# Kernel optimization log

Measured on AMD Instinct MI355X. Metric: run time of the kernel, lower is better.

## Reference

```python
import jax, jax.numpy as jnp
import numpy as np

RESOLUTION = 2 ** 8  # 256
N_POINTS = 2 ** 21


def setup_inputs() -> dict:
    key = jax.random.key(0)
    k1, k2 = jax.random.split(key)
    inp = jax.random.uniform(k1, (N_POINTS, 3), dtype=jnp.float32)
    grid = jax.random.normal(k2, (RESOLUTION, RESOLUTION, RESOLUTION, 3), dtype=jnp.float32) * 0.01
    return {"input": inp, "feature_params": grid}


def reference(input, feature_params):
    R = feature_params.shape[0]
    scaled = input * (R - 1)
    lower = jnp.clip(jnp.floor(scaled).astype(jnp.int32), 0, R - 2)
    upper = jnp.clip(lower + 1, 0, R - 1)
    t = scaled - lower.astype(scaled.dtype)
    xl, yl, zl = lower[:, 0], lower[:, 1], lower[:, 2]
    xu, yu, zu = upper[:, 0], upper[:, 1], upper[:, 2]
    tx, ty, tz = t[:, 0:1], t[:, 1:2], t[:, 2:3]  # (N,1) for broadcast over channels
    # note original indexes grid as [z, y, x]
    c000 = feature_params[zl, yl, xl]
    c001 = feature_params[zl, yl, xu]
    c010 = feature_params[zl, yu, xl]
    c011 = feature_params[zl, yu, xu]
    c100 = feature_params[zu, yl, xl]
    c101 = feature_params[zu, yl, xu]
    c110 = feature_params[zu, yu, xl]
    c111 = feature_params[zu, yu, xu]
    c00 = c000 * (1 - tx) + c001 * tx
    c01 = c010 * (1 - tx) + c011 * tx
    c10 = c100 * (1 - tx) + c101 * tx
    c11 = c110 * (1 - tx) + c111 * tx
    c0 = c00 * (1 - ty) + c01 * ty
    c1 = c10 * (1 - ty) + c11 * ty
    return c0 * (1 - tz) + c1 * tz
```

## Files before the change

kernel.cpp:

```cpp
#include <hip/hip_runtime.h>


#define NB     8192
#define CAP    512u
#define GBLK   512
#define LAYERF4 1728
#define LAYERF  6912
#define GRIDF4  12582912

#define CUR_OFF   67108864u
#define NEEDED    (67108864u + 32768u)

typedef float f4v __attribute__((ext_vector_type(4)));
typedef float f2v __attribute__((ext_vector_type(2)));
typedef f4v f4u __attribute__((aligned(8)));
typedef f2v f2u __attribute__((aligned(8)));

__device__ __forceinline__ void cell_of(float p, int& l, float& t) {
    float s = p * 255.0f;
    int v = (int)floorf(s);
    v = v < 0 ? 0 : (v > 254 ? 254 : v);
    l = v;
    t = s - (float)v;
}

__device__ __forceinline__ int fine_bin3(float px, float py, float pz) {
    int xl, yl, zl; float tx, ty, tz;
    cell_of(px, xl, tx);
    cell_of(py, yl, ty);
    cell_of(pz, zl, tz);
    return (zl << 5) | (yl >> 3);
}

__device__ __forceinline__ void direct_lerp(const float* __restrict__ grid,
                                            float* __restrict__ out, int i,
                                            int xl, int yl, int zl,
                                            float tx, float ty, float tz) {
    int b00 = (zl * 65536 + yl * 256 + xl) * 3;
    int b01 = b00 + 768, b10 = b00 + 196608, b11 = b10 + 768;
    float s00[6], s01[6], s10[6], s11[6];
#pragma unroll
    for (int k = 0; k < 6; ++k) s00[k] = grid[b00 + k];
#pragma unroll
    for (int k = 0; k < 6; ++k) s01[k] = grid[b01 + k];
#pragma unroll
    for (int k = 0; k < 6; ++k) s10[k] = grid[b10 + k];
#pragma unroll
    for (int k = 0; k < 6; ++k) s11[k] = grid[b11 + k];
#pragma unroll
    for (int c = 0; c < 3; ++c) {
        float c00 = s00[c] * (1.0f - tx) + s00[c + 3] * tx;
        float c01 = s01[c] * (1.0f - tx) + s01[c + 3] * tx;
        float c10 = s10[c] * (1.0f - tx) + s10[c + 3] * tx;
        float c11 = s11[c] * (1.0f - tx) + s11[c + 3] * tx;
        float c0 = c00 * (1.0f - ty) + c01 * ty;
        float c1 = c10 * (1.0f - ty) + c11 * ty;
        out[3 * i + c] = c0 * (1.0f - tz) + c1 * tz;
    }
}

__global__ __launch_bounds__(1024) void k_init(unsigned* __restrict__ cur) {
    int i = blockIdx.x * 1024 + threadIdx.x;
    if (i < NB) cur[i] = (unsigned)i * CAP;
}

__global__ __launch_bounds__(1024) void k_scatter(const float* __restrict__ inp,
                                                  const float* __restrict__ grid,
                                                  float4* __restrict__ binned,
                                                  unsigned* __restrict__ cur,
                                                  float* __restrict__ out, int n) {
    __shared__ unsigned cnt[NB];
    __shared__ unsigned base[NB];
    int t = threadIdx.x;
    int P = n >> 1;
    int stride = gridDim.x * 1024;
    int iters = (P + stride - 1) / stride;

    if ((n & 1) && blockIdx.x == 0 && t == 0) {
        int i = n - 1;
        float px = inp[3 * i], py = inp[3 * i + 1], pz = inp[3 * i + 2];
        int b = fine_bin3(px, py, pz);
        unsigned r = atomicAdd(&cur[b], 1u);
        if (r - (unsigned)b * CAP < CAP) {
            float4 v; v.x = px; v.y = py; v.z = pz; v.w = __uint_as_float((unsigned)i);
            binned[r] = v;
        } else {
            int xl, yl, zl; float tx, ty, tz;
            cell_of(px, xl, tx); cell_of(py, yl, ty); cell_of(pz, zl, tz);
            direct_lerp(grid, out, i, xl, yl, zl, tx, ty, tz);
        }
    }

    for (int it = 0; it < iters; ++it) {
        int pr = it * stride + blockIdx.x * 1024 + t;
        for (int k = t; k < NB; k += 1024) cnt[k] = 0;
        __syncthreads();
        int b0 = 0, b1 = 0; unsigned r0 = 0, r1 = 0;
        float4 p0, p1;
        bool valid = (pr < P);
        if (valid) {
            f4v a = *(const f4u*)(inp + 6 * pr);
            f2v b = *(const f2u*)(inp + 6 * pr + 4);
            p0.x = a.x; p0.y = a.y; p0.z = a.z;
            p0.w = __uint_as_float((unsigned)(2 * pr));
            p1.x = a.w; p1.y = b.x; p1.z = b.y;
            p1.w = __uint_as_float((unsigned)(2 * pr + 1));
            b0 = fine_bin3(p0.x, p0.y, p0.z);
            b1 = fine_bin3(p1.x, p1.y, p1.z);
            r0 = atomicAdd(&cnt[b0], 1u);
            r1 = atomicAdd(&cnt[b1], 1u);
        }
        __syncthreads();
        for (int k = t; k < NB; k += 1024)
            if (cnt[k]) base[k] = atomicAdd(&cur[k], cnt[k]);
        __syncthreads();
        if (valid) {
            unsigned s0 = base[b0] + r0;
            unsigned s1 = base[b1] + r1;
            if (s0 - (unsigned)b0 * CAP < CAP) binned[s0] = p0;
            else {
                int xl, yl, zl; float tx, ty, tz;
                cell_of(p0.x, xl, tx); cell_of(p0.y, yl, ty); cell_of(p0.z, zl, tz);
                direct_lerp(grid, out, 2 * pr, xl, yl, zl, tx, ty, tz);
            }
            if (s1 - (unsigned)b1 * CAP < CAP) binned[s1] = p1;
            else {
                int xl, yl, zl; float tx, ty, tz;
                cell_of(p1.x, xl, tx); cell_of(p1.y, yl, ty); cell_of(p1.z, zl, tz);
                direct_lerp(grid, out, 2 * pr + 1, xl, yl, zl, tx, ty, tz);
            }
        }
        __syncthreads();
    }
}

#define LOADL(L)                                                        \
    do {                                                                \
        int zg = z0 + (L); if (zg > 255) zg = 255;                      \
        size_t b4 = (size_t)zg * 49152 + (size_t)y0 * 192;              \
        size_t u0 = b4 + (size_t)t;                                     \
        size_t u1 = b4 + 512 + (size_t)t;                               \
        size_t u2 = b4 + 1024 + (size_t)t;                              \
        if (u0 > (size_t)(GRIDF4 - 1)) u0 = (size_t)(GRIDF4 - 1);       \
        if (u1 > (size_t)(GRIDF4 - 1)) u1 = (size_t)(GRIDF4 - 1);       \
        if (u2 > (size_t)(GRIDF4 - 1)) u2 = (size_t)(GRIDF4 - 1);       \
        R0 = *(const f4u*)(grid + u0 * 4);                              \
        R1 = *(const f4u*)(grid + u1 * 4);                              \
        R2 = *(const f4u*)(grid + u2 * 4);                              \
        if (t < LAYERF4 - 1536) {                                       \
            size_t u3 = b4 + 1536 + (size_t)t;                          \
            if (u3 > (size_t)(GRIDF4 - 1)) u3 = (size_t)(GRIDF4 - 1);   \
            R3 = *(const f4u*)(grid + u3 * 4);                          \
        }                                                               \
    } while (0)

#define WRITEL(slot_)                                                   \
    do {                                                                \
        float* dst = &slab[(slot_) * LAYERF];                           \
        *(f4v*)&dst[(size_t)t * 4] = R0;                                \
        *(f4v*)&dst[(size_t)(t + 512) * 4] = R1;                        \
        *(f4v*)&dst[(size_t)(t + 1024) * 4] = R2;                       \
        if (t < LAYERF4 - 1536) *(f4v*)&dst[(size_t)(t + 1536) * 4] = R3; \
    } while (0)

__global__ __launch_bounds__(GBLK) void k_gather(const float4* __restrict__ binned,
                                                 const float* __restrict__ grid,
                                                 const unsigned* __restrict__ cur,
                                                 float* __restrict__ out) {
    __shared__ __align__(16) float slab[2 * LAYERF];
    int t = threadIdx.x;
    int bin = ((blockIdx.x & 7) << 6) | (blockIdx.x >> 3);
    int zb = bin >> 5;
    int yb = bin & 31;
    int z0 = zb << 4;
    int y0 = yb << 3;

    f4v R0, R1, R2, R3;

    LOADL(0); WRITEL(0);
    LOADL(1);

    for (int zc = 0; zc < 16; ++zc) {
        WRITEL((zc + 1) & 1);
        __syncthreads();

        if (zc <= 14) LOADL(zc + 2);

        int sA = (zc & 1) * LAYERF;
        int sB = ((zc + 1) & 1) * LAYERF;

        int K = ((z0 + zc) << 5) | yb;
        unsigned start = (unsigned)K * CAP;
        unsigned count = cur[K] - start;
        if (count > CAP) count = CAP;

        for (unsigned p = (unsigned)t; p < count; p += (unsigned)GBLK) {
            float4 v = binned[start + p];
            unsigned idx = __float_as_uint(v.w);

            int xl, yl, zl; float tx, ty, tz;
            cell_of(v.x, xl, tx);
            cell_of(v.y, yl, ty);
            cell_of(v.z, zl, tz);
            int row = yl - y0;

            int o00 = sA + row * 768 + xl * 3;
            int o01 = o00 + 768;
            int o10 = sB + row * 768 + xl * 3;
            int o11 = o10 + 768;

#define SEG_READ(b, s)                                   \
            do {                                         \
                int e_ = (b) & ~1;                       \
                bool d_ = ((b) & 1) != 0;                \
                f2v q0 = *(const f2u*)(&slab[e_]);       \
                f2v q1 = *(const f2u*)(&slab[e_ + 2]);   \
                f2v q2 = *(const f2u*)(&slab[e_ + 4]);   \
                f2v q3 = *(const f2u*)(&slab[e_ + 6]);   \
                s[0] = d_ ? q0.y : q0.x;                 \
                s[1] = d_ ? q1.x : q0.y;                 \
                s[2] = d_ ? q1.y : q1.x;                 \
                s[3] = d_ ? q2.x : q1.y;                 \
                s[4] = d_ ? q2.y : q2.x;                 \
                s[5] = d_ ? q3.x : q2.y;                 \
            } while (0)

            float s00[6], s01[6], s10[6], s11[6];
            SEG_READ(o00, s00);
            SEG_READ(o01, s01);
            SEG_READ(o10, s10);
            SEG_READ(o11, s11);
#undef SEG_READ

            float o[3];
#pragma unroll
            for (int c = 0; c < 3; ++c) {
                float c00 = s00[c] * (1.0f - tx) + s00[c + 3] * tx;
                float c01 = s01[c] * (1.0f - tx) + s01[c + 3] * tx;
                float c10 = s10[c] * (1.0f - tx) + s10[c + 3] * tx;
                float c11 = s11[c] * (1.0f - tx) + s11[c + 3] * tx;
                float c0 = c00 * (1.0f - ty) + c01 * ty;
                float c1 = c10 * (1.0f - ty) + c11 * ty;
                o[c] = c0 * (1.0f - tz) + c1 * tz;
            }
            float3 w; w.x = o[0]; w.y = o[1]; w.z = o[2];
            *(float3*)(out + 3 * (size_t)idx) = w;
        }

        __syncthreads();
    }
}

__global__ __launch_bounds__(256) void k_direct(const float* __restrict__ inp,
                                                const float* __restrict__ grid,
                                                float* __restrict__ out, int n) {
    int i = blockIdx.x * blockDim.x + threadIdx.x;
    if (i >= n) return;
    int xl, yl, zl; float tx, ty, tz;
    cell_of(inp[3 * i + 0], xl, tx);
    cell_of(inp[3 * i + 1], yl, ty);
    cell_of(inp[3 * i + 2], zl, tz);
    direct_lerp(grid, out, i, xl, yl, zl, tx, ty, tz);
}

extern "C" void kernel_launch(void* const* d_in, const int* in_sizes, int n_in,
                              void* d_out, int out_size, void* d_ws, size_t ws_size,
                              hipStream_t stream) {
    const float* inp  = (const float*)d_in[0];
    const float* grid = (const float*)d_in[1];
    float* out = (float*)d_out;
    int n = in_sizes[0] / 3;

    if (ws_size < (size_t)NEEDED) {
        int blocks = (n + 255) / 256;
        k_direct<<<blocks, 256, 0, stream>>>(inp, grid, out, n);
        return;
    }

    char* ws = (char*)d_ws;
    float4*   binned = (float4*)ws;
    unsigned* cur    = (unsigned*)(ws + CUR_OFF);

    k_init   <<<8,   1024, 0, stream>>>(cur);
    k_scatter<<<512, 1024, 0, stream>>>(inp, grid, binned, cur, out, n);
    k_gather <<<512, GBLK, 0, stream>>>(binned, grid, cur, out);
}
```

Before: 129.3 us.

## Split gather blocks into two x-halves with smaller shared slabs

Each bin's gather work is split across two blocks, one for each half of the x range. Each block loads only a half-width slab of layers (97 float4 per row over 9 rows) into shared memory and skips points outside its half. This doubles the block count and halves shared memory per block, aiming for more parallelism and occupancy. The cost is that every bin's point list is read twice and cells are recomputed for points that then get skipped.

Result: slower. 161.2 us (+24.7%).

```diff
diff --git a/kernel.cpp b/kernel.cpp
--- a/kernel.cpp
+++ b/kernel.cpp
@@ -4,9 +4,10 @@
 #define NB     8192
 #define CAP    512u
 #define GBLK   512
-#define LAYERF4 1728
-#define LAYERF  6912
-#define GRIDF4  12582912
+#define CHF4   97
+#define LAYF4  873
+#define LAYF   (LAYF4 * 4)
+#define GRIDF4 12582912
 
 #define CUR_OFF   67108864u
 #define NEEDED    (67108864u + 32768u)
@@ -137,45 +138,46 @@
 #define LOADL(L)                                                        \
     do {                                                                \
         int zg = z0 + (L); if (zg > 255) zg = 255;                      \
-        size_t b4 = (size_t)zg * 49152 + (size_t)y0 * 192;              \
-        size_t u0 = b4 + (size_t)t;                                     \
-        size_t u1 = b4 + 512 + (size_t)t;                               \
-        size_t u2 = b4 + 1024 + (size_t)t;                              \
-        if (u0 > (size_t)(GRIDF4 - 1)) u0 = (size_t)(GRIDF4 - 1);       \
-        if (u1 > (size_t)(GRIDF4 - 1)) u1 = (size_t)(GRIDF4 - 1);       \
-        if (u2 > (size_t)(GRIDF4 - 1)) u2 = (size_t)(GRIDF4 - 1);       \
-        R0 = *(const f4u*)(grid + u0 * 4);                              \
-        R1 = *(const f4u*)(grid + u1 * 4);                              \
-        R2 = *(const f4u*)(grid + u2 * 4);                              \
-        if (t < LAYERF4 - 1536) {                                       \
-            size_t u3 = b4 + 1536 + (size_t)t;                          \
-            if (u3 > (size_t)(GRIDF4 - 1)) u3 = (size_t)(GRIDF4 - 1);   \
-            R3 = *(const f4u*)(grid + u3 * 4);                          \
+        size_t b4 = (size_t)zg * 49152 + (size_t)y0 * 192 + (size_t)xq96; \
+        {                                                               \
+            int r_ = t / CHF4, j_ = t - r_ * CHF4;                      \
+            size_t s0_ = b4 + (size_t)r_ * 192 + (size_t)j_;            \
+            if (s0_ > (size_t)(GRIDF4 - 1)) s0_ = (size_t)(GRIDF4 - 1); \
+            R0 = *(const f4u*)(grid + s0_ * 4);                         \
+        }                                                               \
+        if (t < LAYF4 - 512) {                                          \
+            int u_ = t + 512;                                           \
+            int r_ = u_ / CHF4, j_ = u_ - r_ * CHF4;                    \
+            size_t s1_ = b4 + (size_t)r_ * 192 + (size_t)j_;            \
+            if (s1_ > (size_t)(GRIDF4 - 1)) s1_ = (size_t)(GRIDF4 - 1); \
+            R1 = *(const f4u*)(grid + s1_ * 4);                         \
         }                                                               \
     } while (0)
 
 #define WRITEL(slot_)                                                   \
     do {                                                                \
-        float* dst = &slab[(slot_) * LAYERF];                           \
+        float* dst = &slab[(slot_) * LAYF];                             \
         *(f4v*)&dst[(size_t)t * 4] = R0;                                \
-        *(f4v*)&dst[(size_t)(t + 512) * 4] = R1;                        \
-        *(f4v*)&dst[(size_t)(t + 1024) * 4] = R2;                       \
-        if (t < LAYERF4 - 1536) *(f4v*)&dst[(size_t)(t + 1536) * 4] = R3; \
+        if (t < LAYF4 - 512) *(f4v*)&dst[(size_t)(t + 512) * 4] = R1;   \
     } while (0)
 
 __global__ __launch_bounds__(GBLK) void k_gather(const float4* __restrict__ binned,
                                                  const float* __restrict__ grid,
                                                  const unsigned* __restrict__ cur,
                                                  float* __restrict__ out) {
-    __shared__ __align__(16) float slab[2 * LAYERF];
+    __shared__ __align__(16) float slab[2 * LAYF];
     int t = threadIdx.x;
-    int bin = ((blockIdx.x & 7) << 6) | (blockIdx.x >> 3);
+    int col = ((blockIdx.x & 7) << 7) | (blockIdx.x >> 3);
+    int bin = col >> 1;
+    int xh  = col & 1;
     int zb = bin >> 5;
     int yb = bin & 31;
     int z0 = zb << 4;
     int y0 = yb << 3;
-
-    f4v R0, R1, R2, R3;
+    int x0 = xh << 7;
+    int xq96 = xh * 96;
+
+    f4v R0, R1;
 
     LOADL(0); WRITEL(0);
     LOADL(1);
@@ -183,11 +185,10 @@
     for (int zc = 0; zc < 16; ++zc) {
         WRITEL((zc + 1) & 1);
         __syncthreads();
-
         if (zc <= 14) LOADL(zc + 2);
 
-        int sA = (zc & 1) * LAYERF;
-        int sB = ((zc + 1) & 1) * LAYERF;
+        int sA = (zc & 1) * LAYF;
+        int sB = ((zc + 1) & 1) * LAYF;
 
         int K = ((z0 + zc) << 5) | yb;
         unsigned start = (unsigned)K * CAP;
@@ -202,12 +203,15 @@
             cell_of(v.x, xl, tx);
             cell_of(v.y, yl, ty);
             cell_of(v.z, zl, tz);
+            if ((xl >> 7) != xh) continue;
+
             int row = yl - y0;
-
-            int o00 = sA + row * 768 + xl * 3;
-            int o01 = o00 + 768;
-            int o10 = sB + row * 768 + xl * 3;
-            int o11 = o10 + 768;
+            int xc  = xl - x0;
+
+            int o00 = sA + row * 388 + xc * 3;
+            int o01 = o00 + 388;
+            int o10 = sB + row * 388 + xc * 3;
+            int o11 = o10 + 388;
 
 #define SEG_READ(b, s)                                   \
             do {                                         \
@@ -281,7 +285,7 @@
     float4*   binned = (float4*)ws;
     unsigned* cur    = (unsigned*)(ws + CUR_OFF);
 
-    k_init   <<<8,   1024, 0, stream>>>(cur);
-    k_scatter<<<512, 1024, 0, stream>>>(inp, grid, binned, cur, out, n);
-    k_gather <<<512, GBLK, 0, stream>>>(binned, grid, cur, out);
-}
+    k_init   <<<8,    1024, 0, stream>>>(cur);
+    k_scatter<<<512,  1024, 0, stream>>>(inp, grid, binned, cur, out, n);
+    k_gather <<<1024, GBLK, 0, stream>>>(binned, grid, cur, out);
+}
```
